# Performance work log

Measured on AMD Instinct MI355X. Metric: run time of the kernel, lower is better.

Reference implementation:

```python
import jax, jax.numpy as jnp
import numpy as np

EPS = 1e-5   # torch nn.LayerNorm default
H = 12       # num_heads


def layernorm(x, w, b):
    m = jnp.mean(x, axis=-1, keepdims=True)
    v = jnp.var(x, axis=-1, keepdims=True)
    return (x - m) * jax.lax.rsqrt(v + EPS) * w + b


def mha(x, qkv_w, proj_w, proj_b):
    # MemEffAttention math (qkv_bias=False, proj_bias=True), block-diagonal mask
    # over equal-length sequences == independent per-row attention.
    B, N, D = x.shape
    hd = D // H
    qkv = jnp.einsum('bnd,ed->bne', x, qkv_w).reshape(B, N, 3, H, hd)
    q, k, v = qkv[:, :, 0], qkv[:, :, 1], qkv[:, :, 2]
    scale = hd ** -0.5
    attn = jnp.einsum('bnhd,bmhd->bhnm', q * scale, k)     # [B,H,N,N]
    attn = jax.nn.softmax(attn, axis=-1)
    o = jnp.einsum('bhnm,bmhd->bnhd', attn, v).reshape(B, N, D)
    return jnp.einsum('bnd,ed->bne', o, proj_w) + proj_b


def block(x, ln1_w, ln1_b, qkv_w, proj_w, proj_b, ln2_w, ln2_b, fc1_w, fc1_b, fc2_w, fc2_b):
    # x = x + attn(norm1(x)); x = x + mlp(norm2(x))  (ls1/ls2 = Identity, eval mode)
    x = x + mha(layernorm(x, ln1_w, ln1_b), qkv_w, proj_w, proj_b)
    h = layernorm(x, ln2_w, ln2_b)
    h = jax.nn.gelu(jnp.einsum('bnd,ed->bne', h, fc1_w) + fc1_b, approximate=False)
    h = jnp.einsum('bne,de->bnd', h, fc2_w) + fc2_b
    return x + h


def setup_inputs() -> dict:
    key = jax.random.key(0)
    ks = jax.random.split(key, 8)
    D, Dff = 768, 3072
    s = lambda k, shape, sc: jax.random.normal(k, shape, jnp.float32) * sc
    return {
        'x1': s(ks[0], (8, 1370, D), 1.0),
        'x2': s(ks[1], (8, 257, D), 1.0),
        'ln1_w': jnp.ones((D,), jnp.float32), 'ln1_b': jnp.zeros((D,), jnp.float32),
        'qkv_w': s(ks[2], (3 * D, D), 0.02),
        'proj_w': s(ks[3], (D, D), 0.02), 'proj_b': jnp.zeros((D,), jnp.float32),
        'ln2_w': jnp.ones((D,), jnp.float32), 'ln2_b': jnp.zeros((D,), jnp.float32),
        'fc1_w': s(ks[4], (Dff, D), 0.02), 'fc1_b': jnp.zeros((Dff,), jnp.float32),
        'fc2_w': s(ks[5], (D, Dff), 0.02), 'fc2_b': jnp.zeros((D,), jnp.float32),
    }


def reference(x1, x2, ln1_w, ln1_b, qkv_w, proj_w, proj_b, ln2_w, ln2_b,
              fc1_w, fc1_b, fc2_w, fc2_b):
    # forward_nested (eval path): block-diagonal attention over nested groups,
    # which factorizes into per-group batched attention; return the
    # concatenated token stream (same values as attn_bias.split output).
    params = (ln1_w, ln1_b, qkv_w, proj_w, proj_b, ln2_w, ln2_b,
              fc1_w, fc1_b, fc2_w, fc2_b)
    o1 = block(x1, *params)
    o2 = block(x2, *params)
    D = x1.shape[-1]
    return jnp.concatenate([o1.reshape(-1, D), o2.reshape(-1, D)], axis=0)
```

## Files before the change

### kernel.cpp

```cpp
#include <hip/hip_runtime.h>
#include <hip/hip_bf16.h>

typedef __attribute__((ext_vector_type(8))) short bf16x8;
typedef __attribute__((ext_vector_type(4))) float f32x4;
typedef __attribute__((ext_vector_type(16))) float f32x16;

#define GL_LDS16(g, l)                                                        \
  __builtin_amdgcn_global_load_lds((const __attribute__((address_space(1))) void*)(g), \
                                   (__attribute__((address_space(3))) void*)(l), 16, 0, 0)

__device__ __forceinline__ ushort f2bf(float f) {
  union { float f; unsigned u; } x; x.f = f;
  unsigned r = x.u + 0x7fffu + ((x.u >> 16) & 1u);
  return (ushort)(r >> 16);
}

__device__ __forceinline__ float max3f(float a, float b, float c) {
  float d;
  asm("v_max3_f32 %0, %1, %2, %3" : "=v"(d) : "v"(a), "v"(b), "v"(c));
  return d;
}

__device__ __forceinline__ int xcd_remap(int bid, int nwg) {
  int q = nwg >> 3, r = nwg & 7;
  int xcd = bid & 7, idx = bid >> 3;
  return (xcd < r ? xcd * (q + 1) : r * (q + 1) + (xcd - r) * q) + idx;
}

__global__ void cvt_kernel(const float* __restrict__ in, ushort* __restrict__ out, int n) {
  int i = blockIdx.x * blockDim.x + threadIdx.x;
  int stride = gridDim.x * blockDim.x;
  for (; i < n; i += stride) out[i] = f2bf(in[i]);
}

__global__ __launch_bounds__(64) void ln_kernel(
    const float* __restrict__ x1, const float* __restrict__ x2, int M1,
    const float* __restrict__ w, const float* __restrict__ b,
    ushort* __restrict__ out) {
  int row = blockIdx.x;
  int lane = threadIdx.x;
  const float* xr = (row < M1) ? x1 + (size_t)row * 768
                               : x2 + (size_t)(row - M1) * 768;
  float4 v[3];
  float s = 0.f, sq = 0.f;
#pragma unroll
  for (int i = 0; i < 3; i++) {
    v[i] = *(const float4*)(xr + i * 256 + lane * 4);
    s += v[i].x + v[i].y + v[i].z + v[i].w;
    sq += v[i].x * v[i].x + v[i].y * v[i].y + v[i].z * v[i].z + v[i].w * v[i].w;
  }
#pragma unroll
  for (int m = 1; m < 64; m <<= 1) { s += __shfl_xor(s, m); sq += __shfl_xor(sq, m); }
  float mean = s * (1.f / 768.f);
  float var = sq * (1.f / 768.f) - mean * mean;
  float rstd = rsqrtf(var + 1e-5f);
  ushort* orow = out + (size_t)row * 768;
#pragma unroll
  for (int i = 0; i < 3; i++) {
    int d = i * 256 + lane * 4;
    float4 wv = *(const float4*)(w + d);
    float4 bv = *(const float4*)(b + d);
    ushort4 o;
    o.x = f2bf((v[i].x - mean) * rstd * wv.x + bv.x);
    o.y = f2bf((v[i].y - mean) * rstd * wv.y + bv.y);
    o.z = f2bf((v[i].z - mean) * rstd * wv.z + bv.z);
    o.w = f2bf((v[i].w - mean) * rstd * wv.w + bv.w);
    *(ushort4*)(orow + d) = o;
  }
}

template <int MODE>
__global__ __launch_bounds__(256) void gemm_tile(
    const ushort* __restrict__ A, const ushort* __restrict__ W,
    const float* __restrict__ bias, void* __restrict__ outp,
    int M, int N, int K, int ncol) {
  __shared__ ushort lA[128 * 64];
  __shared__ ushort lB[128 * 64];
  const int t = threadIdx.x;
  const int lane = t & 63, wave = t >> 6;
  const int l15 = lane & 15, lg = lane >> 4;
  const int waveM = wave >> 1, waveN = wave & 1;
  const int g = xcd_remap(blockIdx.x, gridDim.x);
  const int rowBlk = (g / ncol) * 128;
  const int colBlk = (g % ncol) * 128;
  const int srow = t >> 3;
  const int schunk = t & 7;

  f32x4 acc[4][4] = {};

  for (int k0 = 0; k0 < K; k0 += 64) {
    if (k0) __syncthreads();
#pragma unroll
    for (int i = 0; i < 4; i++) {
      int row = i * 32 + srow;
      int gch = schunk ^ (row & 7);
      GL_LDS16(A + (size_t)(rowBlk + row) * K + k0 + gch * 8,
               &lA[row * 64 + schunk * 8]);
      GL_LDS16(W + (size_t)(colBlk + row) * K + k0 + gch * 8,
               &lB[row * 64 + schunk * 8]);
    }
    __syncthreads();
#pragma unroll
    for (int kk = 0; kk < 2; kk++) {
      bf16x8 af[4], bfr[4];
#pragma unroll
      for (int m = 0; m < 4; m++) {
        int row = waveM * 64 + m * 16 + l15;
        af[m] = *(const bf16x8*)&lA[row * 64 + ((kk * 32 + lg * 8) ^ ((row & 7) << 3))];
      }
#pragma unroll
      for (int c = 0; c < 4; c++) {
        int row = waveN * 64 + c * 16 + l15;
        bfr[c] = *(const bf16x8*)&lB[row * 64 + ((kk * 32 + lg * 8) ^ ((row & 7) << 3))];
      }
      __builtin_amdgcn_s_setprio(1);
#pragma unroll
      for (int m = 0; m < 4; m++)
#pragma unroll
        for (int c = 0; c < 4; c++)
          acc[m][c] = __builtin_amdgcn_mfma_f32_16x16x32_bf16(af[m], bfr[c], acc[m][c], 0, 0, 0);
      __builtin_amdgcn_s_setprio(0);
    }
  }

  const float qsc = (MODE == 0 && colBlk < 768) ? 0.18033688011112042f : 1.f;
#pragma unroll
  for (int m = 0; m < 4; m++) {
    int rowB = rowBlk + waveM * 64 + m * 16 + lg * 4;
#pragma unroll
    for (int c = 0; c < 4; c++) {
      int col = colBlk + waveN * 64 + c * 16 + l15;
      float bv = (MODE == 2) ? bias[col] : 0.f;
#pragma unroll
      for (int j = 0; j < 4; j++) {
        int r = rowB + j;
        if (r < M) {
          float v = acc[m][c][j] + bv;
          size_t idx = (size_t)r * N + col;
          if (MODE == 2) {
            float gl = 0.5f * v * (1.f + erff(v * 0.70710678118f));
            ((ushort*)outp)[idx] = f2bf(gl);
          } else {
            ((ushort*)outp)[idx] = f2bf(v * qsc);
          }
        }
      }
    }
  }
}

__global__ __launch_bounds__(256) void gemm_tile64(
    const ushort* __restrict__ A, const ushort* __restrict__ W,
    const float* __restrict__ bias, const float* __restrict__ res1,
    const float* __restrict__ res2, int resSplit,
    float* __restrict__ outp, int M, int N, int K, int ncol) {
  __shared__ ushort lA[64 * 64];
  __shared__ ushort lB[128 * 64];
  const int t = threadIdx.x;
  const int lane = t & 63, wave = t >> 6;
  const int l15 = lane & 15, lg = lane >> 4;
  const int waveM = wave >> 1, waveN = wave & 1;
  const int g = xcd_remap(blockIdx.x, gridDim.x);
  const int rowBlk = (g / ncol) * 64;
  const int colBlk = (g % ncol) * 128;
  const int srow = t >> 3;
  const int schunk = t & 7;

  f32x4 acc[2][4] = {};

  for (int k0 = 0; k0 < K; k0 += 64) {
    if (k0) __syncthreads();
#pragma unroll
    for (int i = 0; i < 2; i++) {
      int row = i * 32 + srow;
      int gch = schunk ^ (row & 7);
      GL_LDS16(A + (size_t)(rowBlk + row) * K + k0 + gch * 8,
               &lA[row * 64 + schunk * 8]);
    }
#pragma unroll
    for (int i = 0; i < 4; i++) {
      int row = i * 32 + srow;
      int gch = schunk ^ (row & 7);
      GL_LDS16(W + (size_t)(colBlk + row) * K + k0 + gch * 8,
               &lB[row * 64 + schunk * 8]);
    }
    __syncthreads();
#pragma unroll
    for (int kk = 0; kk < 2; kk++) {
      bf16x8 af[2], bfr[4];
#pragma unroll
      for (int m = 0; m < 2; m++) {
        int row = waveM * 32 + m * 16 + l15;
        af[m] = *(const bf16x8*)&lA[row * 64 + ((kk * 32 + lg * 8) ^ ((row & 7) << 3))];
      }
#pragma unroll
      for (int c = 0; c < 4; c++) {
        int row = waveN * 64 + c * 16 + l15;
        bfr[c] = *(const bf16x8*)&lB[row * 64 + ((kk * 32 + lg * 8) ^ ((row & 7) << 3))];
      }
      __builtin_amdgcn_s_setprio(1);
#pragma unroll
      for (int m = 0; m < 2; m++)
#pragma unroll
        for (int c = 0; c < 4; c++)
          acc[m][c] = __builtin_amdgcn_mfma_f32_16x16x32_bf16(af[m], bfr[c], acc[m][c], 0, 0, 0);
      __builtin_amdgcn_s_setprio(0);
    }
  }

#pragma unroll
  for (int m = 0; m < 2; m++) {
    int rowB = rowBlk + waveM * 32 + m * 16 + lg * 4;
#pragma unroll
    for (int c = 0; c < 4; c++) {
      int col = colBlk + waveN * 64 + c * 16 + l15;
      float bv = bias[col];
#pragma unroll
      for (int j = 0; j < 4; j++) {
        int r = rowB + j;
        if (r < M) {
          size_t idx = (size_t)r * N + col;
          float rv = (r < resSplit) ? res1[idx]
                                    : res2[(size_t)(r - resSplit) * N + col];
          outp[idx] = acc[m][c][j] + bv + rv;
        }
      }
    }
  }
}

__global__ __launch_bounds__(256) void prep_kernel(
    const ushort* __restrict__ qkv, ushort* __restrict__ kt2,
    ushort* __restrict__ vt2, int N1, int N2, int nkv1, int nkv2, int M1) {
  __shared__ ushort lT[64 * 68];
  const int t = threadIdx.x;
  const int kv = blockIdx.x;
  const int bhg = blockIdx.y;
  const int part = bhg >= 96;
  const int bh = part ? bhg - 96 : bhg;
  const int N = part ? N2 : N1;
  const int nkv = part ? nkv2 : nkv1;
  if (kv >= nkv) return;
  const size_t rowbase = part ? (size_t)M1 : 0;
  const int b = bh / 12, h = bh % 12;
  const int k0 = kv * 64;
  const ushort* Kp = qkv + (rowbase + (size_t)b * N) * 2304 + 768 + h * 64;
  const ushort* Vp = Kp + 768;
  size_t tbase = (part ? (size_t)96 * nkv1 : 0) + (size_t)bh * nkv + kv;
  ushort* ktile = kt2 + tbase * 4096;
  ushort* vtile = vt2 + tbase * 4096;
#pragma unroll
  for (int p = 0; p < 2; p++) {
    int s = p * 256 + t;
    int chunk = s >> 6, krow = s & 63;
    ushort4 v0 = {0, 0, 0, 0}, v1 = {0, 0, 0, 0};
    if (k0 + krow < N) {
      const ushort* src = Kp + (size_t)(k0 + krow) * 2304 + chunk * 8;
      v0 = *(const ushort4*)src;
      v1 = *(const ushort4*)(src + 4);
    }
    *(ushort4*)&ktile[s * 8] = v0;
    *(ushort4*)&ktile[s * 8 + 4] = v1;
  }
#pragma unroll
  for (int p = 0; p < 2; p++) {
    int nl = p * 32 + (t >> 3);
    int dc = t & 7;
    ushort4 v0 = {0, 0, 0, 0}, v1 = {0, 0, 0, 0};
    if (k0 + nl < N) {
      const ushort* src = Vp + (size_t)(k0 + nl) * 2304 + dc * 8;
      v0 = *(const ushort4*)src;
      v1 = *(const ushort4*)(src + 4);
    }
    *(ushort4*)&lT[nl * 68 + dc * 8] = v0;
    *(ushort4*)&lT[nl * 68 + dc * 8 + 4] = v1;
  }
  __syncthreads();
#pragma unroll
  for (int p = 0; p < 2; p++) {
    int s = p * 256 + t;
    int kchunk = s >> 6, d = s & 63;
    ushort o[8];
#pragma unroll
    for (int j = 0; j < 8; j++) o[j] = lT[(kchunk * 8 + j) * 68 + d];
    *(ushort4*)&vtile[s * 8] = *(ushort4*)o;
    *(ushort4*)&vtile[s * 8 + 4] = *(ushort4*)(o + 4);
  }
}

#define ATTN_STAGE(buf, kvi)                                                   \
  do {                                                                         \
    _Pragma("unroll") for (int p = 0; p < 2; p++) {                            \
      int s = p * 256 + t;                                                     \
      GL_LDS16(tK + (size_t)(kvi) * 4096 + s * 8, &lK[buf][s * 8]);            \
      GL_LDS16(tV + (size_t)(kvi) * 4096 + s * 8, &lV[buf][s * 8]);            \
    }                                                                          \
  } while (0)

__global__ __launch_bounds__(256) void attn_kernel(
    const ushort* __restrict__ qkv, const ushort* __restrict__ kt2,
    const ushort* __restrict__ vt2, ushort* __restrict__ o_out,
    int N1, int N2, int nkv1, int nkv2, int M1) {
  __shared__ ushort lK[2][4096];
  __shared__ ushort lV[2][4096];
  const int t = threadIdx.x;
  const int lane = t & 63, wave = t >> 6;
  const int l31 = lane & 31, hi = lane >> 5;
  const int bhg = blockIdx.y;
  const int part = bhg >= 96;
  const int bh = part ? bhg - 96 : bhg;
  const int N = part ? N2 : N1;
  const int nkv = part ? nkv2 : nkv1;
  const int qb = blockIdx.x * 128;
  if (qb >= N) return;
  const size_t rowbase = part ? (size_t)M1 : 0;
  const int b = bh / 12, h = bh % 12;
  const ushort* Qp = qkv + (rowbase + (size_t)b * N) * 2304 + h * 64;
  const size_t tboff = (part ? (size_t)96 * nkv1 : 0) + (size_t)bh * nkv;
  const ushort* tK = kt2 + tboff * 4096;
  const ushort* tV = vt2 + tboff * 4096;

  const int qrow = min(qb + wave * 32 + l31, N - 1);
  bf16x8 qf[4];
#pragma unroll
  for (int kc = 0; kc < 4; kc++)
    qf[kc] = *(const bf16x8*)(Qp + (size_t)qrow * 2304 + kc * 16 + hi * 8);

  union { unsigned u[4]; bf16x8 v; } ones;
#pragma unroll
  for (int i = 0; i < 4; i++) ones.u[i] = 0x3F803F80u;

  f32x16 oacc[2] = {};
  f32x16 osum = {};
  float mrun = -1e30f;

  ATTN_STAGE(0, 0);
  __syncthreads();
  for (int kv = 0; kv < nkv; kv++) {
    int cur = kv & 1;
    if (kv + 1 < nkv) ATTN_STAGE(cur ^ 1, kv + 1);
    const bool fullTile = (kv * 64 + 64 <= N);
    f32x16 sacc0 = {}, sacc1 = {};
    __builtin_amdgcn_s_setprio(1);
#pragma unroll
    for (int kc = 0; kc < 4; kc++) {
      bf16x8 kf0 = *(const bf16x8*)&lK[cur][(((kc * 2 + hi) << 6) + l31) * 8];
      bf16x8 kf1 = *(const bf16x8*)&lK[cur][(((kc * 2 + hi) << 6) + 32 + l31) * 8];
      sacc0 = __builtin_amdgcn_mfma_f32_32x32x16_bf16(kf0, qf[kc], sacc0, 0, 0, 0);
      sacc1 = __builtin_amdgcn_mfma_f32_32x32x16_bf16(kf1, qf[kc], sacc1, 0, 0, 0);
    }
    __builtin_amdgcn_s_setprio(0);
    float z[32];
#pragma unroll
    for (int r = 0; r < 16; r++) { z[r] = sacc0[r]; z[16 + r] = sacc1[r]; }
    if (!fullTile) {
#pragma unroll
      for (int i = 0; i < 32; i++) {
        int kg = kv * 64 + (i >> 4) * 32 + (i & 3) + (((i & 15) >> 2) << 3) + (hi << 2);
        if (kg >= N) z[i] = -1e30f;
      }
    }
    float mA[11];
#pragma unroll
    for (int i = 0; i < 10; i++) mA[i] = max3f(z[3 * i], z[3 * i + 1], z[3 * i + 2]);
    mA[10] = fmaxf(z[30], z[31]);
    float mB[4];
#pragma unroll
    for (int i = 0; i < 3; i++) mB[i] = max3f(mA[3 * i], mA[3 * i + 1], mA[3 * i + 2]);
    mB[3] = fmaxf(mA[9], mA[10]);
    float mx = fmaxf(max3f(mB[0], mB[1], mB[2]), mB[3]);
    {
      float a = mx, bx = mx;
      asm("v_permlane32_swap_b32 %0, %1" : "+&v"(a), "+v"(bx));
      mx = fmaxf(a, bx);
    }
    if (!__all(mx <= mrun + 8.f)) {
      float mnew = fmaxf(mrun, mx);
      float corr = exp2f(mrun - mnew);
      oacc[0] *= corr;
      oacc[1] *= corr;
      osum *= corr;
      mrun = mnew;
    }
#pragma unroll
    for (int i = 0; i < 32; i++) z[i] = exp2f(z[i] - mrun);
#pragma unroll
    for (int kt = 0; kt < 2; kt++) {
      unsigned w0[4], w1[4];
#pragma unroll
      for (int rr = 0; rr < 4; rr++) {
        asm("v_cvt_pk_bf16_f32 %0, %1, %2" : "=v"(w0[rr]) : "v"(z[kt * 16 + 4 * rr]), "v"(z[kt * 16 + 4 * rr + 1]));
        asm("v_cvt_pk_bf16_f32 %0, %1, %2" : "=v"(w1[rr]) : "v"(z[kt * 16 + 4 * rr + 2]), "v"(z[kt * 16 + 4 * rr + 3]));
      }
#pragma unroll
      for (int kc2 = 0; kc2 < 2; kc2++) {
        unsigned ua = w0[2 * kc2], ub = w0[2 * kc2 + 1];
        unsigned uc = w1[2 * kc2], ud = w1[2 * kc2 + 1];
        asm("v_permlane32_swap_b32 %0, %1" : "+&v"(ua), "+v"(ub));
        asm("v_permlane32_swap_b32 %0, %1" : "+&v"(uc), "+v"(ud));
        union { unsigned u[4]; bf16x8 v; } pa;
        pa.u[0] = ua; pa.u[1] = uc; pa.u[2] = ub; pa.u[3] = ud;
        int kcg = kt * 2 + kc2;
        __builtin_amdgcn_s_setprio(1);
#pragma unroll
        for (int dt = 0; dt < 2; dt++) {
          bf16x8 vf = *(const bf16x8*)&lV[cur][(((kcg * 2 + hi) << 6) + dt * 32 + l31) * 8];
          oacc[dt] = __builtin_amdgcn_mfma_f32_32x32x16_bf16(pa.v, vf, oacc[dt], 0, 0, 0);
        }
        osum = __builtin_amdgcn_mfma_f32_32x32x16_bf16(pa.v, ones.v, osum, 0, 0, 0);
        __builtin_amdgcn_s_setprio(0);
      }
    }
    __syncthreads();
  }
#pragma unroll
  for (int r = 0; r < 16; r++) {
    int q = qb + wave * 32 + (r & 3) + ((r >> 2) << 3) + (hi << 2);
    if (q < N) {
      float inv;
      asm("v_rcp_f32 %0, %1" : "=v"(inv) : "v"(osum[r]));
      ushort* orow = o_out + (rowbase + (size_t)b * N + q) * 768 + h * 64;
      orow[l31] = f2bf(oacc[0][r] * inv);
      orow[32 + l31] = f2bf(oacc[1][r] * inv);
    }
  }
}

extern "C" void kernel_launch(void* const* d_in, const int* in_sizes, int n_in,
                              void* d_out, int out_size, void* d_ws, size_t ws_size,
                              hipStream_t stream) {
  const float* x1 = (const float*)d_in[0];
  const float* x2 = (const float*)d_in[1];
  const float* ln1_w = (const float*)d_in[2];
  const float* ln1_b = (const float*)d_in[3];
  const float* qkv_w = (const float*)d_in[4];
  const float* proj_w = (const float*)d_in[5];
  const float* proj_b = (const float*)d_in[6];
  const float* ln2_w = (const float*)d_in[7];
  const float* ln2_b = (const float*)d_in[8];
  const float* fc1_w = (const float*)d_in[9];
  const float* fc1_b = (const float*)d_in[10];
  const float* fc2_w = (const float*)d_in[11];
  const float* fc2_b = (const float*)d_in[12];
  float* out = (float*)d_out;

  const int N1 = 1370, N2 = 257;
  const int M1 = 8 * N1, M2 = 8 * N2;
  const int MT = M1 + M2;
  const int MPAD = 13056;
  const int nkv1 = 22, nkv2 = 5;

  char* ws = (char*)d_ws;
  ushort* wq = (ushort*)ws;   ws += (size_t)2304 * 768 * 2;
  ushort* wp = (ushort*)ws;   ws += (size_t)768 * 768 * 2;
  ushort* w1 = (ushort*)ws;   ws += (size_t)3072 * 768 * 2;
  ushort* w2 = (ushort*)ws;   ws += (size_t)768 * 3072 * 2;
  ushort* bufA = (ushort*)ws;   ws += (size_t)MPAD * 768 * 2;
  ushort* bufQKV = (ushort*)ws; ws += (size_t)MPAD * 2304 * 2;
  ushort* bufFF = (ushort*)ws;  ws += (size_t)MPAD * 3072 * 2;
  const size_t nTiles = (size_t)96 * (nkv1 + nkv2);
  ushort* kt2 = bufFF;
  ushort* vt2 = bufFF + nTiles * 4096;

  cvt_kernel<<<2048, 256, 0, stream>>>(qkv_w, wq, 2304 * 768);
  cvt_kernel<<<2048, 256, 0, stream>>>(proj_w, wp, 768 * 768);
  cvt_kernel<<<2048, 256, 0, stream>>>(fc1_w, w1, 3072 * 768);
  cvt_kernel<<<2048, 256, 0, stream>>>(fc2_w, w2, 768 * 3072);

  ln_kernel<<<MT, 64, 0, stream>>>(x1, x2, M1, ln1_w, ln1_b, bufA);
  gemm_tile<0><<<(MPAD / 128) * 18, 256, 0, stream>>>(
      bufA, wq, nullptr, bufQKV, MT, 2304, 768, 18);
  prep_kernel<<<dim3(nkv1, 192), 256, 0, stream>>>(bufQKV, kt2, vt2, N1, N2, nkv1, nkv2, M1);
  attn_kernel<<<dim3(11, 192), 256, 0, stream>>>(
      bufQKV, kt2, vt2, bufA, N1, N2, nkv1, nkv2, M1);
  gemm_tile64<<<(MPAD / 64) * 6, 256, 0, stream>>>(
      bufA, wp, proj_b, x1, x2, M1, out, MT, 768, 768, 6);
  ln_kernel<<<MT, 64, 0, stream>>>(out, out, MT, ln2_w, ln2_b, bufA);
  gemm_tile<2><<<(MPAD / 128) * 24, 256, 0, stream>>>(
      bufA, w1, fc1_b, bufFF, MT, 3072, 768, 24);
  gemm_tile64<<<(MPAD / 64) * 6, 256, 0, stream>>>(
      bufFF, w2, fc2_b, out, nullptr, MT, out, MT, 768, 3072, 6);
}
```

Before: 488.3 us.

## Merge weight conversions, pack four LN rows per block, swap attention grid axes

The four fp32-to-bf16 weight conversion launches become one kernel that walks all four weights into a contiguous workspace, cutting launch count. LayerNorm now packs four rows (one per wave) into each 256-thread block instead of one 64-thread block per row. The prep and attention grids swap axes so head/batch index is the fast-varying block dimension, which changes the order blocks are scheduled and how the many early-exit blocks of the short-sequence part are spread. The single conversion kernel relies on wq, wp, w1, w2 being laid out back to back in the workspace.

```diff
diff --git a/kernel.cpp b/kernel.cpp
--- a/kernel.cpp
+++ b/kernel.cpp
@@ -27,18 +27,30 @@
   return (xcd < r ? xcd * (q + 1) : r * (q + 1) + (xcd - r) * q) + idx;
 }
 
-__global__ void cvt_kernel(const float* __restrict__ in, ushort* __restrict__ out, int n) {
+__global__ void cvt4_kernel(const float* __restrict__ i0, const float* __restrict__ i1,
+                            const float* __restrict__ i2, const float* __restrict__ i3,
+                            int n0, int n1, int n2, int n3,
+                            ushort* __restrict__ out) {
+  int c1 = n0, c2 = n0 + n1, c3 = n0 + n1 + n2, nt = n0 + n1 + n2 + n3;
   int i = blockIdx.x * blockDim.x + threadIdx.x;
   int stride = gridDim.x * blockDim.x;
-  for (; i < n; i += stride) out[i] = f2bf(in[i]);
-}
-
-__global__ __launch_bounds__(64) void ln_kernel(
-    const float* __restrict__ x1, const float* __restrict__ x2, int M1,
+  for (; i < nt; i += stride) {
+    float v;
+    if (i < c1) v = i0[i];
+    else if (i < c2) v = i1[i - c1];
+    else if (i < c3) v = i2[i - c2];
+    else v = i3[i - c3];
+    out[i] = f2bf(v);
+  }
+}
+
+__global__ __launch_bounds__(256) void ln_kernel(
+    const float* __restrict__ x1, const float* __restrict__ x2, int M1, int MT,
     const float* __restrict__ w, const float* __restrict__ b,
     ushort* __restrict__ out) {
-  int row = blockIdx.x;
-  int lane = threadIdx.x;
+  int row = blockIdx.x * 4 + (threadIdx.x >> 6);
+  if (row >= MT) return;
+  int lane = threadIdx.x & 63;
   const float* xr = (row < M1) ? x1 + (size_t)row * 768
                                : x2 + (size_t)(row - M1) * 768;
   float4 v[3];
@@ -234,8 +246,8 @@
     ushort* __restrict__ vt2, int N1, int N2, int nkv1, int nkv2, int M1) {
   __shared__ ushort lT[64 * 68];
   const int t = threadIdx.x;
-  const int kv = blockIdx.x;
-  const int bhg = blockIdx.y;
+  const int bhg = blockIdx.x;
+  const int kv = blockIdx.y;
   const int part = bhg >= 96;
   const int bh = part ? bhg - 96 : bhg;
   const int N = part ? N2 : N1;
@@ -306,12 +318,12 @@
   const int t = threadIdx.x;
   const int lane = t & 63, wave = t >> 6;
   const int l31 = lane & 31, hi = lane >> 5;
-  const int bhg = blockIdx.y;
+  const int bhg = blockIdx.x;
   const int part = bhg >= 96;
   const int bh = part ? bhg - 96 : bhg;
   const int N = part ? N2 : N1;
   const int nkv = part ? nkv2 : nkv1;
-  const int qb = blockIdx.x * 128;
+  const int qb = blockIdx.y * 128;
   if (qb >= N) return;
   const size_t rowbase = part ? (size_t)M1 : 0;
   const int b = bh / 12, h = bh % 12;
@@ -462,20 +474,18 @@
   ushort* kt2 = bufFF;
   ushort* vt2 = bufFF + nTiles * 4096;
 
-  cvt_kernel<<<2048, 256, 0, stream>>>(qkv_w, wq, 2304 * 768);
-  cvt_kernel<<<2048, 256, 0, stream>>>(proj_w, wp, 768 * 768);
-  cvt_kernel<<<2048, 256, 0, stream>>>(fc1_w, w1, 3072 * 768);
-  cvt_kernel<<<2048, 256, 0, stream>>>(fc2_w, w2, 768 * 3072);
-
-  ln_kernel<<<MT, 64, 0, stream>>>(x1, x2, M1, ln1_w, ln1_b, bufA);
+  cvt4_kernel<<<2048, 256, 0, stream>>>(qkv_w, proj_w, fc1_w, fc2_w,
+                                        2304 * 768, 768 * 768, 3072 * 768, 768 * 3072, wq);
+
+  ln_kernel<<<(MT + 3) / 4, 256, 0, stream>>>(x1, x2, M1, MT, ln1_w, ln1_b, bufA);
   gemm_tile<0><<<(MPAD / 128) * 18, 256, 0, stream>>>(
       bufA, wq, nullptr, bufQKV, MT, 2304, 768, 18);
-  prep_kernel<<<dim3(nkv1, 192), 256, 0, stream>>>(bufQKV, kt2, vt2, N1, N2, nkv1, nkv2, M1);
-  attn_kernel<<<dim3(11, 192), 256, 0, stream>>>(
+  prep_kernel<<<dim3(192, nkv1), 256, 0, stream>>>(bufQKV, kt2, vt2, N1, N2, nkv1, nkv2, M1);
+  attn_kernel<<<dim3(192, 11), 256, 0, stream>>>(
       bufQKV, kt2, vt2, bufA, N1, N2, nkv1, nkv2, M1);
   gemm_tile64<<<(MPAD / 64) * 6, 256, 0, stream>>>(
       bufA, wp, proj_b, x1, x2, M1, out, MT, 768, 768, 6);
-  ln_kernel<<<MT, 64, 0, stream>>>(out, out, MT, ln2_w, ln2_b, bufA);
+  ln_kernel<<<(MT + 3) / 4, 256, 0, stream>>>(out, out, MT, MT, ln2_w, ln2_b, bufA);
   gemm_tile<2><<<(MPAD / 128) * 24, 256, 0, stream>>>(
       bufA, w1, fc1_b, bufFF, MT, 3072, 768, 24);
   gemm_tile64<<<(MPAD / 64) * 6, 256, 0, stream>>>(
```

Measured after the change: 479.3 us. No clear change (-1.9%).
